# Performance work log

Hardware: AMD Instinct MI355X
Metric: run time of the kernel (lower is better)

The kernel has to match this reference:

```python
import jax, jax.numpy as jnp
import numpy as np

B, T, NLAT, N, D = 8, 4, 64, 2048, 1024
HEADS, HEAD_DIM = 16, 64
ADIM = HEADS * HEAD_DIM
EPS = 1e-5


def layer_norm(x, w, b):
    mu = jnp.mean(x, axis=-1, keepdims=True)
    var = jnp.var(x, axis=-1, keepdims=True)
    return (x - mu) * jax.lax.rsqrt(var + EPS) * w + b


def setup_inputs() -> dict:
    key = jax.random.key(0)
    ks = jax.random.split(key, 8)
    s = 0.02
    return {
        "latents": jax.random.normal(ks[0], (B, T, NLAT, D), jnp.float32),
        "x": jax.random.normal(ks[1], (B, T, N, D), jnp.float32),
        "Wq": jax.random.normal(ks[2], (D, ADIM), jnp.float32) * s,     # [in, out]
        "Wkv": jax.random.normal(ks[3], (D, 2 * ADIM), jnp.float32) * s,
        "Wout": jax.random.normal(ks[4], (ADIM, D), jnp.float32) * s,
        "bout": jnp.zeros((D,), jnp.float32),
        "lnl_w": jnp.ones((D,), jnp.float32),
        "lnl_b": jnp.zeros((D,), jnp.float32),
        "lnm_w": jnp.ones((D,), jnp.float32),
        "lnm_b": jnp.zeros((D,), jnp.float32),
    }


def reference(latents, x, Wq, Wkv, Wout, bout, lnl_w, lnl_b, lnm_w, lnm_b):
    scale = HEAD_DIM ** (-0.5)
    lat = layer_norm(latents, lnl_w, lnl_b)          # [B,T,NLAT,D]
    med = layer_norm(x, lnm_w, lnm_b)                # [B,T,N,D]
    q = lat @ Wq                                      # [B,T,NLAT,ADIM]
    kv_in = jnp.concatenate((med, lat), axis=-2)      # [B,T,N+NLAT,D]
    kv = kv_in @ Wkv                                  # [B,T,N+NLAT,2*ADIM]
    k, v = jnp.split(kv, 2, axis=-1)
    # split heads: b t n (h d) -> b h t n d
    def split_heads(z):
        b, t, n, _ = z.shape
        return z.reshape(b, t, n, HEADS, HEAD_DIM).transpose(0, 3, 1, 2, 4)
    q = split_heads(q) * scale
    k = split_heads(k)
    v = split_heads(v)
    scores = jnp.einsum('bhtid,bhtjd->bhtij', q, k)   # [B,H,T,NLAT,N+NLAT]
    attn = jax.nn.softmax(scores, axis=-1)            # max-subtract handled internally
    out = jnp.einsum('bhtij,bhtjd->bhtid', attn, v)   # [B,H,T,NLAT,HEAD_DIM]
    out = out.transpose(0, 2, 3, 1, 4).reshape(B, T, NLAT, ADIM)
    return out @ Wout + bout
```

## Files before the change

kernel.cpp:

```cpp
#include <hip/hip_runtime.h>
#include <hip/hip_bf16.h>
#include <stdint.h>

#define B_    8
#define T_    4
#define NLAT  64
#define NMED  2048
#define NKV   2112
#define D_    1024
#define HEADS 16
#define HD    64
#define ADIM  1024
#define BT    32

#define GK    1024
#define GN    2048
#define GM    67584
#define MT2   264
#define NSLC  32

typedef __attribute__((ext_vector_type(8))) short bf16x8;
typedef __attribute__((ext_vector_type(4))) float f32x4;

__device__ __forceinline__ ushort f2bf(float f) {
  union { float f; uint32_t u; } v; v.f = f;
  return (ushort)((v.u + 0x7fff + ((v.u >> 16) & 1)) >> 16);
}

__device__ __forceinline__ void gload_lds16(const void* g, void* l) {
  __builtin_amdgcn_global_load_lds(
      (const __attribute__((address_space(1))) void*)g,
      (__attribute__((address_space(3))) void*)l, 16, 0, 0);
}

__device__ __forceinline__ f32x4 mfma16(bf16x8 a, bf16x8 b, f32x4 c) {
  return __builtin_amdgcn_mfma_f32_16x16x32_bf16(a, b, c, 0, 0, 0);
}

__global__ __launch_bounds__(256) void wtrans(const float* __restrict__ src,
                                              ushort* __restrict__ dst,
                                              int K, int Nm) {
  __shared__ float t[64][65];
  const int tr = blockIdx.y, tc = blockIdx.x;
  const int c = threadIdx.x & 63;
  const int r4 = threadIdx.x >> 6;
#pragma unroll
  for (int rr = 0; rr < 16; ++rr) {
    int r = r4 + rr * 4;
    t[r][c] = src[(size_t)(tr * 64 + r) * Nm + tc * 64 + c];
  }
  __syncthreads();
#pragma unroll
  for (int rr = 0; rr < 16; ++rr) {
    int n = r4 + rr * 4;
    dst[(size_t)(tc * 64 + n) * K + tr * 64 + c] = f2bf(t[c][n]);
  }
}

__global__ __launch_bounds__(256) void ln_kernel(
    const float* __restrict__ lat, const float* __restrict__ x,
    const float* __restrict__ lnl_w, const float* __restrict__ lnl_b,
    const float* __restrict__ lnm_w, const float* __restrict__ lnm_b,
    ushort* __restrict__ kvin) {
  const int row = blockIdx.x;
  const int bt = row / NKV;
  const int j = row - bt * NKV;
  const float* src;
  const float* w;
  const float* bb;
  if (j < NMED) {
    src = x + ((size_t)bt * NMED + j) * D_;
    w = lnm_w; bb = lnm_b;
  } else {
    src = lat + ((size_t)bt * NLAT + (j - NMED)) * D_;
    w = lnl_w; bb = lnl_b;
  }
  const int tid = threadIdx.x;
  float4 v = ((const float4*)src)[tid];
  float s = v.x + v.y + v.z + v.w;
  float s2 = v.x * v.x + v.y * v.y + v.z * v.z + v.w * v.w;
#pragma unroll
  for (int off = 1; off < 64; off <<= 1) {
    s += __shfl_xor(s, off, 64);
    s2 += __shfl_xor(s2, off, 64);
  }
  __shared__ float red[8];
  const int wave = tid >> 6;
  if ((tid & 63) == 0) { red[wave] = s; red[4 + wave] = s2; }
  __syncthreads();
  float S = red[0] + red[1] + red[2] + red[3];
  float S2 = red[4] + red[5] + red[6] + red[7];
  const float inv = 1.f / (float)D_;
  float mu = S * inv;
  float var = S2 * inv - mu * mu;
  float rs = rsqrtf(var + 1e-5f);
  float4 wv = ((const float4*)w)[tid];
  float4 bv = ((const float4*)bb)[tid];
  ushort4 ov;
  ov.x = f2bf((v.x - mu) * rs * wv.x + bv.x);
  ov.y = f2bf((v.y - mu) * rs * wv.y + bv.y);
  ov.z = f2bf((v.z - mu) * rs * wv.z + bv.z);
  ov.w = f2bf((v.w - mu) * rs * wv.w + bv.w);
  ((ushort4*)(kvin + (size_t)row * D_))[tid] = ov;
}

template <int AMODE, int OUTMODE>
__global__ __launch_bounds__(256, 3) void gemm128(const ushort* __restrict__ A,
                                                  const ushort* __restrict__ Bt,
                                                  void* __restrict__ C,
                                                  const float* __restrict__ bias,
                                                  int ntx, int nwg, int K, int ldc) {
  __shared__ ushort lsA[128 * 32];
  __shared__ ushort lsB[128 * 32];
  const int tid = threadIdx.x;
  const int lane = tid & 63;
  const int wave = tid >> 6;
  const int lr = lane & 15;
  const int lg = lane >> 4;
  const int wr = (wave >> 1) * 64;
  const int wc = (wave & 1) * 64;

  const int g = blockIdx.x;
  const int cpx = nwg >> 3;
  const int v = (g & 7) * cpx + (g >> 3);
  const int bx = v % ntx;
  const int by = v / ntx;
  const long brow = (long)by * 128;
  const int bcol = bx * 128;

  const int pcx = lg ^ ((lr >> 1) & 3);

  f32x4 acc[4][4];
#pragma unroll
  for (int m = 0; m < 4; ++m)
#pragma unroll
    for (int n = 0; n < 4; ++n) acc[m][n] = (f32x4){0.f, 0.f, 0.f, 0.f};

  const int s0 = tid, s1 = 256 + tid;
  const int r0 = s0 >> 2, r1 = s1 >> 2;
  const int c0 = (s0 & 3) ^ ((s0 >> 3) & 3);
  const int c1 = (s1 & 3) ^ ((s1 >> 3) & 3);
  const int o0 = (s0 & ~63) * 16;
  const int o1 = (s1 & ~63) * 16;

  long arow0, arow1;
  if (AMODE == 1) {
    int g0 = (int)brow + r0, g1 = (int)brow + r1;
    arow0 = (long)(g0 >> 6) * NKV + NMED + (g0 & 63);
    arow1 = (long)(g1 >> 6) * NKV + NMED + (g1 & 63);
  } else {
    arow0 = brow + r0;
    arow1 = brow + r1;
  }
  const long browB0 = (long)(bcol + r0) * K;
  const long browB1 = (long)(bcol + r1) * K;

  for (int k0 = 0; k0 < K; k0 += 32) {
    gload_lds16(A + arow0 * (long)K + k0 + c0 * 8, (char*)lsA + o0);
    gload_lds16(A + arow1 * (long)K + k0 + c1 * 8, (char*)lsA + o1);
    gload_lds16(Bt + browB0 + k0 + c0 * 8, (char*)lsB + o0);
    gload_lds16(Bt + browB1 + k0 + c1 * 8, (char*)lsB + o1);
    __syncthreads();

    bf16x8 af[4], bf[4];
#pragma unroll
    for (int m = 0; m < 4; ++m)
      af[m] = *(const bf16x8*)((char*)lsA + (wr + m * 16 + lr) * 64 + pcx * 16);
#pragma unroll
    for (int n = 0; n < 4; ++n)
      bf[n] = *(const bf16x8*)((char*)lsB + (wc + n * 16 + lr) * 64 + pcx * 16);
#pragma unroll
    for (int m = 0; m < 4; ++m)
#pragma unroll
      for (int n = 0; n < 4; ++n)
        acc[m][n] = mfma16(bf[n], af[m], acc[m][n]);
    __syncthreads();
  }

#pragma unroll
  for (int m = 0; m < 4; ++m) {
    long row = brow + wr + m * 16 + lr;
#pragma unroll
    for (int n = 0; n < 4; ++n) {
      int coln = bcol + wc + n * 16 + lg * 4;
      long off = row * (long)ldc + coln;
      if (OUTMODE == 2) {
        float4 bv = *(const float4*)(bias + coln);
        float4 o;
        o.x = acc[m][n][0] + bv.x;
        o.y = acc[m][n][1] + bv.y;
        o.z = acc[m][n][2] + bv.z;
        o.w = acc[m][n][3] + bv.w;
        *(float4*)((float*)C + off) = o;
      } else {
        const float sc = (OUTMODE == 1) ? 0.125f : 1.f;
        ushort4 o;
        o.x = f2bf(acc[m][n][0] * sc);
        o.y = f2bf(acc[m][n][1] * sc);
        o.z = f2bf(acc[m][n][2] * sc);
        o.w = f2bf(acc[m][n][3] * sc);
        *(ushort4*)((ushort*)C + off) = o;
      }
    }
  }
}

__global__ __launch_bounds__(512, 2) void gemm256(const ushort* __restrict__ A,
                                                  const ushort* __restrict__ Bt,
                                                  ushort* __restrict__ C) {
  extern __shared__ __align__(16) char smem[];
  const int tid = threadIdx.x;
  const int lane = tid & 63;
  const int wv = tid >> 6;
  const int wm = wv >> 2;
  const int wn = wv & 3;
  const int lr = lane & 15;
  const int lg = lane >> 4;

  const int g = blockIdx.x;
  const int v = (g & 7) * MT2 + (g >> 3);
  const int bx = v & 7;
  const int by = v >> 3;
  const long brow = (long)by * 256;
  const int bcol = bx * 256;

  const int pcx = lg ^ ((lr >> 1) & 3);
  const int rbA = wm * 128 + lr;
  const int rbB = wn * 64 + lr;

  f32x4 acc[8][4];
#pragma unroll
  for (int m = 0; m < 8; ++m)
#pragma unroll
    for (int n = 0; n < 4; ++n) acc[m][n] = (f32x4){0.f, 0.f, 0.f, 0.f};

  const int s0 = tid, s1 = 512 + tid;
  const int r0 = s0 >> 2, r1 = s1 >> 2;
  const int c0 = (s0 & 3) ^ ((s0 >> 3) & 3);
  const int c1 = (s1 & 3) ^ ((s1 >> 3) & 3);
  const int o0 = (s0 & ~63) * 16;
  const int o1 = (s1 & ~63) * 16;

#define STAGE_A(slc, slot)                                                     \
  {                                                                            \
    long k0 = (long)(slc) * 32;                                                \
    char* db = smem + (slot) * 32768;                                          \
    gload_lds16(A + (brow + r0) * (long)GK + k0 + c0 * 8, db + o0);            \
    gload_lds16(A + (brow + r1) * (long)GK + k0 + c1 * 8, db + o1);            \
  }
#define STAGE_B(slc, slot)                                                     \
  {                                                                            \
    long k0 = (long)(slc) * 32;                                                \
    char* db = smem + (slot) * 32768 + 16384;                                  \
    gload_lds16(Bt + (long)(bcol + r0) * GK + k0 + c0 * 8, db + o0);           \
    gload_lds16(Bt + (long)(bcol + r1) * GK + k0 + c1 * 8, db + o1);           \
  }

  bf16x8 a0[4], a1[4], b0[4], b1[4];

  STAGE_A(0, 0); STAGE_B(0, 0);
  STAGE_A(1, 1); STAGE_B(1, 1);
  STAGE_A(2, 2); STAGE_B(2, 2);
  asm volatile("s_waitcnt vmcnt(8)" ::: "memory");
  __builtin_amdgcn_s_barrier();
#pragma unroll
  for (int m = 0; m < 4; ++m)
    a0[m] = *(const bf16x8*)(smem + (rbA + m * 16) * 64 + pcx * 16);
#pragma unroll
  for (int n = 0; n < 4; ++n)
    b0[n] = *(const bf16x8*)(smem + 16384 + (rbB + n * 16) * 64 + pcx * 16);
  __builtin_amdgcn_sched_barrier(0);

#define SLICE(T, BCUR, BNXT)                                                   \
  {                                                                            \
    const int t_ = (T);                                                        \
    const char* sA_ = smem + (t_ & 3) * 32768;                                 \
    const int ts_ = (t_ + 3 < NSLC) ? t_ + 3 : t_;                             \
    const int ws_ = (t_ + 3) & 3;                                              \
                                                        \
    _Pragma("unroll")                                                          \
    for (int m = 0; m < 4; ++m)                                                \
      a1[m] = *(const bf16x8*)(sA_ + (rbA + (m + 4) * 16) * 64 + pcx * 16);    \
    STAGE_A(ts_, ws_);                                                         \
    __builtin_amdgcn_sched_barrier(0);                                         \
    __builtin_amdgcn_s_barrier();                                              \
    asm volatile("s_waitcnt lgkmcnt(4)" ::: "memory");                         \
    __builtin_amdgcn_sched_barrier(0);                                         \
    __builtin_amdgcn_s_setprio(1);                                             \
    _Pragma("unroll")                                                          \
    for (int m = 0; m < 4; ++m)                                                \
      _Pragma("unroll")                                                        \
      for (int n = 0; n < 4; ++n)                                              \
        acc[m][n] = mfma16(BCUR[n], a0[m], acc[m][n]);                         \
    __builtin_amdgcn_s_setprio(0);                                             \
    __builtin_amdgcn_sched_barrier(0);                                         \
    __builtin_amdgcn_s_barrier();                                              \
                                                        \
    STAGE_B(ts_, ws_);                                                         \
    asm volatile("s_waitcnt vmcnt(8)" ::: "memory");                           \
    __builtin_amdgcn_sched_barrier(0);                                         \
    __builtin_amdgcn_s_barrier();                                              \
    {                                                                          \
      const int tn_ = (t_ + 1 < NSLC) ? t_ + 1 : t_;                           \
      const char* nA_ = smem + (tn_ & 3) * 32768;                              \
      const char* nB_ = nA_ + 16384;                                           \
      _Pragma("unroll")                                                        \
      for (int m = 0; m < 4; ++m)                                              \
        a0[m] = *(const bf16x8*)(nA_ + (rbA + m * 16) * 64 + pcx * 16);        \
      _Pragma("unroll")                                                        \
      for (int n = 0; n < 4; ++n)                                              \
        BNXT[n] = *(const bf16x8*)(nB_ + (rbB + n * 16) * 64 + pcx * 16);      \
    }                                                                          \
    __builtin_amdgcn_sched_barrier(0);                                         \
    asm volatile("s_waitcnt lgkmcnt(8)" ::: "memory");                         \
    __builtin_amdgcn_sched_barrier(0);                                         \
    __builtin_amdgcn_s_setprio(1);                                             \
    _Pragma("unroll")                                                          \
    for (int m = 0; m < 4; ++m)                                                \
      _Pragma("unroll")                                                        \
      for (int n = 0; n < 4; ++n)                                              \
        acc[m + 4][n] = mfma16(BCUR[n], a1[m], acc[m + 4][n]);                 \
    __builtin_amdgcn_s_setprio(0);                                             \
    __builtin_amdgcn_sched_barrier(0);                                         \
    __builtin_amdgcn_s_barrier();                                              \
  }

  for (int t = 0; t < NSLC; t += 2) {
    SLICE(t, b0, b1);
    SLICE(t + 1, b1, b0);
  }
#undef SLICE
#undef STAGE_A
#undef STAGE_B

#pragma unroll
  for (int m = 0; m < 8; ++m) {
    long row = brow + wm * 128 + m * 16 + lr;
    ushort* crow = C + row * GN + bcol + wn * 64 + lg * 4;
#pragma unroll
    for (int n = 0; n < 4; ++n) {
      ushort4 o;
      o.x = f2bf(acc[m][n][0]);
      o.y = f2bf(acc[m][n][1]);
      o.z = f2bf(acc[m][n][2]);
      o.w = f2bf(acc[m][n][3]);
      *(ushort4*)(crow + n * 16) = o;
    }
  }
}

__global__ __launch_bounds__(256) void attn_kernel(const ushort* __restrict__ q,
                                                   const ushort* __restrict__ kv,
                                                   ushort* __restrict__ o) {
  const int blk = blockIdx.x;
  const int bt = blk >> 4;
  const int h = blk & 15;
  const int tid = threadIdx.x;
  const int wave = tid >> 6;
  const int lane = tid & 63;
  const int lr = lane & 15;
  const int lg = lane >> 4;

  __shared__ ushort vt[64][72];
  __shared__ ushort pl[4][16][72];
  __shared__ ushort kl[64 * 64];

  const ushort* qbase = q + (size_t)(bt * 64 + wave * 16) * ADIM + h * HD;
  bf16x8 qf[2];
#pragma unroll
  for (int ks = 0; ks < 2; ++ks)
    qf[ks] = *(const bf16x8*)(qbase + (size_t)lr * ADIM + ks * 32 + lg * 8);

  const ushort* kvb = kv + (size_t)bt * NKV * 2048;
  const int jj = tid >> 2;
  const int q4 = tid & 3;

  f32x4 accO[4];
#pragma unroll
  for (int n = 0; n < 4; ++n) accO[n] = (f32x4){0.f, 0.f, 0.f, 0.f};
  float mrun[4] = {-1e30f, -1e30f, -1e30f, -1e30f};
  float lrun[4] = {0.f, 0.f, 0.f, 0.f};

  bf16x8 kr0, kr1, vr0, vr1;
  {
    const ushort* src = kvb + (size_t)jj * 2048 + h * HD + q4 * 16;
    kr0 = *(const bf16x8*)(src);
    kr1 = *(const bf16x8*)(src + 8);
    vr0 = *(const bf16x8*)(src + ADIM);
    vr1 = *(const bf16x8*)(src + ADIM + 8);
  }

  for (int jt = 0; jt < NKV / 64; ++jt) {
    __syncthreads();

    {
      int p0 = (q4 * 2) ^ (jj & 7);
      int p1 = (q4 * 2 + 1) ^ (jj & 7);
      *(bf16x8*)((char*)kl + jj * 128 + p0 * 16) = kr0;
      *(bf16x8*)((char*)kl + jj * 128 + p1 * 16) = kr1;
      int d0 = q4 * 16;
#pragma unroll
      for (int e = 0; e < 8; ++e) {
        vt[d0 + e][jj] = ((const ushort*)&vr0)[e];
        vt[d0 + 8 + e][jj] = ((const ushort*)&vr1)[e];
      }
    }

    bf16x8 nk0, nk1, nv0, nv1;
    {
      const int tn = (jt + 1 < NKV / 64) ? jt + 1 : jt;
      const ushort* src = kvb + (size_t)(tn * 64 + jj) * 2048 + h * HD + q4 * 16;
      nk0 = *(const bf16x8*)(src);
      nk1 = *(const bf16x8*)(src + 8);
      nv0 = *(const bf16x8*)(src + ADIM);
      nv1 = *(const bf16x8*)(src + ADIM + 8);
    }
    __syncthreads();

    f32x4 s[4];
#pragma unroll
    for (int nj = 0; nj < 4; ++nj) s[nj] = (f32x4){0.f, 0.f, 0.f, 0.f};
#pragma unroll
    for (int nj = 0; nj < 4; ++nj)
#pragma unroll
      for (int ks = 0; ks < 2; ++ks) {
        int row = nj * 16 + lr;
        int phys = (4 * ks + lg) ^ (lr & 7);
        bf16x8 kf = *(const bf16x8*)((char*)kl + row * 128 + phys * 16);
        s[nj] = mfma16(qf[ks], kf, s[nj]);
      }

    float mt[4], corr[4], psum[4];
#pragma unroll
    for (int r = 0; r < 4; ++r)
      mt[r] = fmaxf(fmaxf(s[0][r], s[1][r]), fmaxf(s[2][r], s[3][r]));
#pragma unroll
    for (int off = 1; off < 16; off <<= 1)
#pragma unroll
      for (int r = 0; r < 4; ++r) mt[r] = fmaxf(mt[r], __shfl_xor(mt[r], off, 64));
#pragma unroll
    for (int r = 0; r < 4; ++r) {
      float mn = fmaxf(mrun[r], mt[r]);
      corr[r] = __expf(mrun[r] - mn);
      mrun[r] = mn;
      psum[r] = 0.f;
    }
#pragma unroll
    for (int nj = 0; nj < 4; ++nj)
#pragma unroll
      for (int r = 0; r < 4; ++r) {
        float pv = __expf(s[nj][r] - mrun[r]);
        s[nj][r] = pv;
        psum[r] += pv;
      }
#pragma unroll
    for (int off = 1; off < 16; off <<= 1)
#pragma unroll
      for (int r = 0; r < 4; ++r) psum[r] += __shfl_xor(psum[r], off, 64);
#pragma unroll
    for (int r = 0; r < 4; ++r) lrun[r] = lrun[r] * corr[r] + psum[r];
#pragma unroll
    for (int n = 0; n < 4; ++n)
#pragma unroll
      for (int r = 0; r < 4; ++r) accO[n][r] *= corr[r];

#pragma unroll
    for (int nj = 0; nj < 4; ++nj)
#pragma unroll
      for (int r = 0; r < 4; ++r)
        pl[wave][lg * 4 + r][nj * 16 + lr] = f2bf(s[nj][r]);
    __syncthreads();

    bf16x8 pf[2];
#pragma unroll
    for (int ks = 0; ks < 2; ++ks)
      pf[ks] = *(const bf16x8*)&pl[wave][lr][ks * 32 + lg * 8];
#pragma unroll
    for (int nd = 0; nd < 4; ++nd)
#pragma unroll
      for (int ks = 0; ks < 2; ++ks) {
        bf16x8 vf = *(const bf16x8*)&vt[nd * 16 + lr][ks * 32 + lg * 8];
        accO[nd] = mfma16(pf[ks], vf, accO[nd]);
      }

    kr0 = nk0; kr1 = nk1; vr0 = nv0; vr1 = nv1;
  }

#pragma unroll
  for (int nd = 0; nd < 4; ++nd)
#pragma unroll
    for (int r = 0; r < 4; ++r) {
      float vv = accO[nd][r] / lrun[r];
      int row = bt * 64 + wave * 16 + lg * 4 + r;
      o[(size_t)row * ADIM + h * HD + nd * 16 + lr] = f2bf(vv);
    }
}

extern "C" void kernel_launch(void* const* d_in, const int* in_sizes, int n_in,
                              void* d_out, int out_size, void* d_ws, size_t ws_size,
                              hipStream_t stream) {
  const float* latents = (const float*)d_in[0];
  const float* x = (const float*)d_in[1];
  const float* Wq = (const float*)d_in[2];
  const float* Wkv = (const float*)d_in[3];
  const float* Wout = (const float*)d_in[4];
  const float* bout = (const float*)d_in[5];
  const float* lnl_w = (const float*)d_in[6];
  const float* lnl_b = (const float*)d_in[7];
  const float* lnm_w = (const float*)d_in[8];
  const float* lnm_b = (const float*)d_in[9];

  char* ws = (char*)d_ws;
  size_t off = 0;
  auto alloc = [&](size_t bytes) -> void* {
    void* p = ws + off;
    off += (bytes + 255) & ~(size_t)255;
    return p;
  };
  ushort* kvin = (ushort*)alloc((size_t)BT * NKV * D_ * 2);
  ushort* kvo  = (ushort*)alloc((size_t)BT * NKV * 2048 * 2);
  ushort* qb   = (ushort*)alloc((size_t)BT * NLAT * ADIM * 2);
  ushort* ao   = (ushort*)alloc((size_t)BT * NLAT * ADIM * 2);
  ushort* WqT  = (ushort*)alloc((size_t)D_ * ADIM * 2);
  ushort* WkvT = (ushort*)alloc((size_t)D_ * 2 * ADIM * 2);
  ushort* WoutT = (ushort*)alloc((size_t)ADIM * D_ * 2);

  hipFuncSetAttribute((const void*)gemm256,
                      hipFuncAttributeMaxDynamicSharedMemorySize, 131072);

  wtrans<<<dim3(ADIM / 64, D_ / 64), 256, 0, stream>>>(Wq, WqT, D_, ADIM);
  wtrans<<<dim3(2 * ADIM / 64, D_ / 64), 256, 0, stream>>>(Wkv, WkvT, D_, 2 * ADIM);
  wtrans<<<dim3(D_ / 64, ADIM / 64), 256, 0, stream>>>(Wout, WoutT, ADIM, D_);

  ln_kernel<<<BT * NKV, 256, 0, stream>>>(latents, x, lnl_w, lnl_b, lnm_w, lnm_b, kvin);

  gemm128<1, 1><<<dim3(128), 256, 0, stream>>>(
      kvin, WqT, qb, nullptr, ADIM / 128, 128, D_, ADIM);

  gemm256<<<dim3(MT2 * 8), 512, 131072, stream>>>(kvin, WkvT, kvo);

  attn_kernel<<<BT * HEADS, 256, 0, stream>>>(qb, kvo, ao);

  gemm128<0, 2><<<dim3(128), 256, 0, stream>>>(
      ao, WoutT, d_out, bout, D_ / 128, 128, ADIM, D_);
}
```

Measured before the change: 555.5 us.

## Fuse Q projection into KV GEMM launch and transpose attention score layout

```diff
diff --git a/kernel.cpp b/kernel.cpp
--- a/kernel.cpp
+++ b/kernel.cpp
@@ -16,8 +16,8 @@
 #define GK    1024
 #define GN    2048
 #define GM    67584
-#define MT2   264
 #define NSLC  32
+#define NWG_BIG 2144
 
 typedef __attribute__((ext_vector_type(8))) short bf16x8;
 typedef __attribute__((ext_vector_type(4))) float f32x4;
@@ -206,8 +206,10 @@
 }
 
 __global__ __launch_bounds__(512, 2) void gemm256(const ushort* __restrict__ A,
-                                                  const ushort* __restrict__ Bt,
-                                                  ushort* __restrict__ C) {
+                                                  const ushort* __restrict__ BtKV,
+                                                  const ushort* __restrict__ BtQ,
+                                                  ushort* __restrict__ Ckv,
+                                                  ushort* __restrict__ Cq) {
   extern __shared__ __align__(16) char smem[];
   const int tid = threadIdx.x;
   const int lane = tid & 63;
@@ -218,11 +220,21 @@
   const int lg = lane >> 4;
 
   const int g = blockIdx.x;
-  const int v = (g & 7) * MT2 + (g >> 3);
-  const int bx = v & 7;
-  const int by = v >> 3;
-  const long brow = (long)by * 256;
-  const int bcol = bx * 256;
+  const int v = (g & 7) * (NWG_BIG / 8) + (g >> 3);
+  const bool isq = v >= 2112;
+  long brow; int bcol;
+  const ushort* Bp; ushort* Cp; int ldc;
+  if (!isq) {
+    brow = (long)(v >> 3) * 256;
+    bcol = (v & 7) * 256;
+    Bp = BtKV; Cp = Ckv; ldc = GN;
+  } else {
+    int u = v - 2112;
+    brow = (long)(u >> 2) * 256;
+    bcol = (u & 3) * 256;
+    Bp = BtQ; Cp = Cq; ldc = ADIM;
+  }
+  const float sc = isq ? 0.125f : 1.f;
 
   const int pcx = lg ^ ((lr >> 1) & 3);
   const int rbA = wm * 128 + lr;
@@ -241,19 +253,29 @@
   const int o0 = (s0 & ~63) * 16;
   const int o1 = (s1 & ~63) * 16;
 
+  long arow0, arow1;
+  if (isq) {
+    int g0 = (int)brow + r0, g1 = (int)brow + r1;
+    arow0 = (long)(g0 >> 6) * NKV + NMED + (g0 & 63);
+    arow1 = (long)(g1 >> 6) * NKV + NMED + (g1 & 63);
+  } else {
+    arow0 = brow + r0;
+    arow1 = brow + r1;
+  }
+
 #define STAGE_A(slc, slot)                                                     \
   {                                                                            \
     long k0 = (long)(slc) * 32;                                                \
     char* db = smem + (slot) * 32768;                                          \
-    gload_lds16(A + (brow + r0) * (long)GK + k0 + c0 * 8, db + o0);            \
-    gload_lds16(A + (brow + r1) * (long)GK + k0 + c1 * 8, db + o1);            \
+    gload_lds16(A + arow0 * (long)GK + k0 + c0 * 8, db + o0);                  \
+    gload_lds16(A + arow1 * (long)GK + k0 + c1 * 8, db + o1);                  \
   }
 #define STAGE_B(slc, slot)                                                     \
   {                                                                            \
     long k0 = (long)(slc) * 32;                                                \
     char* db = smem + (slot) * 32768 + 16384;                                  \
-    gload_lds16(Bt + (long)(bcol + r0) * GK + k0 + c0 * 8, db + o0);           \
-    gload_lds16(Bt + (long)(bcol + r1) * GK + k0 + c1 * 8, db + o1);           \
+    gload_lds16(Bp + (long)(bcol + r0) * GK + k0 + c0 * 8, db + o0);           \
+    gload_lds16(Bp + (long)(bcol + r1) * GK + k0 + c1 * 8, db + o1);           \
   }
 
   bf16x8 a0[4], a1[4], b0[4], b1[4];
@@ -336,14 +358,14 @@
 #pragma unroll
   for (int m = 0; m < 8; ++m) {
     long row = brow + wm * 128 + m * 16 + lr;
-    ushort* crow = C + row * GN + bcol + wn * 64 + lg * 4;
+    ushort* crow = Cp + row * ldc + bcol + wn * 64 + lg * 4;
 #pragma unroll
     for (int n = 0; n < 4; ++n) {
       ushort4 o;
-      o.x = f2bf(acc[m][n][0]);
-      o.y = f2bf(acc[m][n][1]);
-      o.z = f2bf(acc[m][n][2]);
-      o.w = f2bf(acc[m][n][3]);
+      o.x = f2bf(acc[m][n][0] * sc);
+      o.y = f2bf(acc[m][n][1] * sc);
+      o.z = f2bf(acc[m][n][2] * sc);
+      o.w = f2bf(acc[m][n][3] * sc);
       *(ushort4*)(crow + n * 16) = o;
     }
   }
@@ -361,7 +383,7 @@
   const int lr = lane & 15;
   const int lg = lane >> 4;
 
-  __shared__ ushort vt[64][72];
+  __shared__ ushort vtf[64 * 72];
   __shared__ ushort pl[4][16][72];
   __shared__ ushort kl[64 * 64];
 
@@ -378,8 +400,8 @@
   f32x4 accO[4];
 #pragma unroll
   for (int n = 0; n < 4; ++n) accO[n] = (f32x4){0.f, 0.f, 0.f, 0.f};
-  float mrun[4] = {-1e30f, -1e30f, -1e30f, -1e30f};
-  float lrun[4] = {0.f, 0.f, 0.f, 0.f};
+  float mrun = -1e30f;
+  float lrun = 0.f;
 
   bf16x8 kr0, kr1, vr0, vr1;
   {
@@ -399,10 +421,11 @@
       *(bf16x8*)((char*)kl + jj * 128 + p0 * 16) = kr0;
       *(bf16x8*)((char*)kl + jj * 128 + p1 * 16) = kr1;
       int d0 = q4 * 16;
+      int jc = jj >> 3, jb = jj & 7;
 #pragma unroll
       for (int e = 0; e < 8; ++e) {
-        vt[d0 + e][jj] = ((const ushort*)&vr0)[e];
-        vt[d0 + 8 + e][jj] = ((const ushort*)&vr1)[e];
+        vtf[(d0 + e) * 72 + (jc ^ (e & 7)) * 8 + jb] = ((const ushort*)&vr0)[e];
+        vtf[(d0 + 8 + e) * 72 + (jc ^ (e & 7)) * 8 + jb] = ((const ushort*)&vr1)[e];
       }
     }
 
@@ -427,48 +450,44 @@
         int row = nj * 16 + lr;
         int phys = (4 * ks + lg) ^ (lr & 7);
         bf16x8 kf = *(const bf16x8*)((char*)kl + row * 128 + phys * 16);
-        s[nj] = mfma16(qf[ks], kf, s[nj]);
+        s[nj] = mfma16(kf, qf[ks], s[nj]);
       }
 
-    float mt[4], corr[4], psum[4];
-#pragma unroll
-    for (int r = 0; r < 4; ++r)
-      mt[r] = fmaxf(fmaxf(s[0][r], s[1][r]), fmaxf(s[2][r], s[3][r]));
-#pragma unroll
-    for (int off = 1; off < 16; off <<= 1)
-#pragma unroll
-      for (int r = 0; r < 4; ++r) mt[r] = fmaxf(mt[r], __shfl_xor(mt[r], off, 64));
-#pragma unroll
-    for (int r = 0; r < 4; ++r) {
-      float mn = fmaxf(mrun[r], mt[r]);
-      corr[r] = __expf(mrun[r] - mn);
-      mrun[r] = mn;
-      psum[r] = 0.f;
-    }
+    float mloc = s[0][0];
 #pragma unroll
     for (int nj = 0; nj < 4; ++nj)
 #pragma unroll
+      for (int r = 0; r < 4; ++r) mloc = fmaxf(mloc, s[nj][r]);
+    mloc = fmaxf(mloc, __shfl_xor(mloc, 16, 64));
+    mloc = fmaxf(mloc, __shfl_xor(mloc, 32, 64));
+    float mn = fmaxf(mrun, mloc);
+    float corr = __expf(mrun - mn);
+    mrun = mn;
+    float ps = 0.f;
+#pragma unroll
+    for (int nj = 0; nj < 4; ++nj)
+#pragma unroll
       for (int r = 0; r < 4; ++r) {
-        float pv = __expf(s[nj][r] - mrun[r]);
+        float pv = __expf(s[nj][r] - mn);
         s[nj][r] = pv;
-        psum[r] += pv;
+        ps += pv;
       }
-#pragma unroll
-    for (int off = 1; off < 16; off <<= 1)
-#pragma unroll
-      for (int r = 0; r < 4; ++r) psum[r] += __shfl_xor(psum[r], off, 64);
-#pragma unroll
-    for (int r = 0; r < 4; ++r) lrun[r] = lrun[r] * corr[r] + psum[r];
+    ps += __shfl_xor(ps, 16, 64);
+    ps += __shfl_xor(ps, 32, 64);
+    lrun = lrun * corr + ps;
+    float corrq[4];
+#pragma unroll
+    for (int r = 0; r < 4; ++r) corrq[r] = __shfl(corr, lg * 4 + r, 64);
 #pragma unroll
     for (int n = 0; n < 4; ++n)
 #pragma unroll
-      for (int r = 0; r < 4; ++r) accO[n][r] *= corr[r];
+      for (int r = 0; r < 4; ++r) accO[n][r] *= corrq[r];
 
 #pragma unroll
     for (int nj = 0; nj < 4; ++nj)
 #pragma unroll
       for (int r = 0; r < 4; ++r)
-        pl[wave][lg * 4 + r][nj * 16 + lr] = f2bf(s[nj][r]);
+        pl[wave][lr][nj * 16 + 4 * lg + r] = f2bf(s[nj][r]);
     __syncthreads();
 
     bf16x8 pf[2];
@@ -479,18 +498,22 @@
     for (int nd = 0; nd < 4; ++nd)
 #pragma unroll
       for (int ks = 0; ks < 2; ++ks) {
-        bf16x8 vf = *(const bf16x8*)&vt[nd * 16 + lr][ks * 32 + lg * 8];
+        bf16x8 vf = *(const bf16x8*)&vtf[(nd * 16 + lr) * 72 +
+                                         ((4 * ks + lg) ^ (lr & 7)) * 8];
         accO[nd] = mfma16(pf[ks], vf, accO[nd]);
       }
 
     kr0 = nk0; kr1 = nk1; vr0 = nv0; vr1 = nv1;
   }
 
+  float lq[4];
+#pragma unroll
+  for (int r = 0; r < 4; ++r) lq[r] = __shfl(lrun, lg * 4 + r, 64);
 #pragma unroll
   for (int nd = 0; nd < 4; ++nd)
 #pragma unroll
     for (int r = 0; r < 4; ++r) {
-      float vv = accO[nd][r] / lrun[r];
+      float vv = accO[nd][r] / lq[r];
       int row = bt * 64 + wave * 16 + lg * 4 + r;
       o[(size_t)row * ADIM + h * HD + nd * 16 + lr] = f2bf(vv);
     }
@@ -534,10 +557,7 @@
 
   ln_kernel<<<BT * NKV, 256, 0, stream>>>(latents, x, lnl_w, lnl_b, lnm_w, lnm_b, kvin);
 
-  gemm128<1, 1><<<dim3(128), 256, 0, stream>>>(
-      kvin, WqT, qb, nullptr, ADIM / 128, 128, D_, ADIM);
-
-  gemm256<<<dim3(MT2 * 8), 512, 131072, stream>>>(kvin, WkvT, kvo);
+  gemm256<<<dim3(NWG_BIG), 512, 131072, stream>>>(kvin, WkvT, WqT, kvo, qb);
 
   attn_kernel<<<BT * HEADS, 256, 0, stream>>>(qb, kvo, ao);
 
```

Measured after the change: 521.8 us. 6.1% less time.
